# Kernel optimization log

Measured on AMD Instinct MI355X. Metric: run time of the kernel, lower is better.

The kernel has to match this reference:

```python
import jax, jax.numpy as jnp
import numpy as np

FRAC_BIT = 12
SCALE = float(2 ** FRAC_BIT)          # 12 fractional bits
QMIN, QMAX = -32768.0, 32767.0        # signed 16-bit two's complement range


def quant16(x):
    """Quantize to signed 16-bit fixed point with 12 fractional bits.

    Matches float_to_16bits_tensor / bit_slice semantics: the bit-serial
    crossbar MVM of the sliced operands equals an exact integer product of
    these fixed-point values, rescaled back to float.
    """
    return jnp.clip(jnp.round(x * SCALE), QMIN, QMAX) / SCALE


def setup_inputs() -> dict:
    key = jax.random.key(0)
    k1, k2 = jax.random.split(key)
    x = jax.random.normal(k1, (32, 128, 56, 56), dtype=jnp.float32)
    # kaiming-ish scale so weights are well inside the fixed-point range
    weight = jax.random.normal(k2, (256, 128, 3, 3), dtype=jnp.float32) * 0.05
    return {"x": x, "weight": weight}


def reference(x, weight):
    # The nested i/j loop in the original slides a stride-1 window over the
    # zero-padded input, performing a bit-sliced crossbar MVM per pixel.
    # That is exactly conv2d(stride=1, padding=1) on 16-bit fixed-point
    # quantized input and weight (bias row in the crossbar is zero / unused).
    qx = quant16(x)
    qw = quant16(weight)
    out = jax.lax.conv_general_dilated(
        qx, qw,
        window_strides=(1, 1),
        padding=((1, 1), (1, 1)),
        dimension_numbers=("NCHW", "OIHW", "NCHW"),
    )
    return out
```

## Files before the change

kernel.cpp:

```cpp
#include <hip/hip_runtime.h>
#include <cstdint>
#include <cstddef>


typedef __attribute__((ext_vector_type(8))) short short8;
typedef __attribute__((ext_vector_type(4))) float floatx4;

#define NIMG 32
#define CIN  128
#define HW   56
#define KOUT 256
#define HP   58
#define XPAD_ELEMS ((size_t)NIMG * HP * HP * CIN)
#define WT_OFF_BYTES (XPAD_ELEMS * 2)
#define KK 1152

__device__ __forceinline__ uint16_t quant_bf16(float v) {
    float q = rintf(v * 4096.0f);
    q = fminf(fmaxf(q, -32768.0f), 32767.0f) * (1.0f / 4096.0f);
    union { float f; uint32_t u; } cv; cv.f = q;
    uint32_t u = cv.u;
    return (uint16_t)((u + 0x7fffu + ((u >> 16) & 1u)) >> 16);
}

__global__ __launch_bounds__(256) void quant_pad_x(const float* __restrict__ x,
                                                   uint16_t* __restrict__ xp) {
    const int b = blockIdx.x;
    const int n = b / HW, h = b - n * HW;
    __shared__ uint16_t tile[HW * 130];
    const float* src = x + (size_t)n * CIN * HW * HW + (size_t)h * HW;
    for (int t = threadIdx.x; t < CIN * HW; t += 256) {
        int c = t / HW, w = t - c * HW;
        tile[w * 130 + c] = quant_bf16(src[(size_t)c * (HW * HW) + w]);
    }
    __syncthreads();
    uint32_t* dst = (uint32_t*)(xp + ((size_t)(n * HP + h + 1) * HP + 1) * CIN);
    for (int t = threadIdx.x; t < (HW * CIN) / 2; t += 256) {
        int w = t >> 6;
        int c2 = t & 63;
        uint32_t lo = tile[w * 130 + c2 * 2];
        uint32_t hi = tile[w * 130 + c2 * 2 + 1];
        dst[t] = lo | (hi << 16);
    }
}

__global__ __launch_bounds__(256) void quant_w(const float* __restrict__ w,
                                               uint16_t* __restrict__ wt) {
    int i = blockIdx.x * 256 + threadIdx.x;
    int k = i / KK;
    int r = i - k * KK;
    int tap = r >> 7;
    int c = r & 127;
    wt[i] = quant_bf16(w[(size_t)(k * CIN + c) * 9 + tap]);
}

__global__ __launch_bounds__(256) void conv_gemm(const uint16_t* __restrict__ xp,
                                                 const uint16_t* __restrict__ wt,
                                                 float* __restrict__ out) {
    __shared__ __align__(16) uint16_t As[128 * 32];
    __shared__ __align__(16) uint16_t Bs[128 * 32];

    const int tid = threadIdx.x;
    const int l   = tid & 63;
    const int wv  = tid >> 6;
    const int wr  = wv >> 1;
    const int wc  = wv & 1;
    const int kblk  = blockIdx.x;
    const int pxblk = blockIdx.y;

    const int chunk = l & 3;
    const int sub   = l >> 2;

    const uint16_t* aG[2];
    const uint16_t* bG[2];
#pragma unroll
    for (int i = 0; i < 2; ++i) {
        int row = wv * 32 + i * 16 + sub;
        aG[i] = wt + (size_t)(kblk * 128 + row) * KK + chunk * 8;
        int p = pxblk * 128 + row;
        int n = p / 3136; int rem = p - n * 3136;
        int hh = rem / HW; int ww = rem - hh * HW;
        bG[i] = xp + (size_t)((n * HP + hh) * HP + ww) * CIN + chunk * 8;
    }

    floatx4 acc[4][4];
#pragma unroll
    for (int a = 0; a < 4; ++a)
#pragma unroll
        for (int b = 0; b < 4; ++b)
            acc[a][b] = (floatx4){0.f, 0.f, 0.f, 0.f};

    const int m16 = l & 15;
    const int q   = l >> 4;

    for (int tap = 0; tap < 9; ++tap) {
        const int toff = (tap / 3) * HP + (tap % 3);
#pragma unroll
        for (int c4 = 0; c4 < 4; ++c4) {
            const int kt = tap * 4 + c4;
#pragma unroll
            for (int i = 0; i < 2; ++i) {
                __builtin_amdgcn_global_load_lds(
                    (__attribute__((address_space(1))) void*)(void*)(aG[i] + kt * 32),
                    (__attribute__((address_space(3))) void*)(void*)(&As[wv * 1024 + i * 512]),
                    16, 0, 0);
                __builtin_amdgcn_global_load_lds(
                    (__attribute__((address_space(1))) void*)(void*)(bG[i] + toff * CIN + c4 * 32),
                    (__attribute__((address_space(3))) void*)(void*)(&Bs[wv * 1024 + i * 512]),
                    16, 0, 0);
            }
            __syncthreads();
            short8 af[4], bf[4];
#pragma unroll
            for (int f = 0; f < 4; ++f) {
                af[f] = *(const short8*)&As[(wr * 64 + f * 16 + m16) * 32 + q * 8];
                bf[f] = *(const short8*)&Bs[(wc * 64 + f * 16 + m16) * 32 + q * 8];
            }
#pragma unroll
            for (int fr = 0; fr < 4; ++fr)
#pragma unroll
                for (int fc = 0; fc < 4; ++fc)
                    acc[fr][fc] = __builtin_amdgcn_mfma_f32_16x16x32_bf16(
                        af[fr], bf[fc], acc[fr][fc], 0, 0, 0);
            __syncthreads();
        }
    }

#pragma unroll
    for (int fc = 0; fc < 4; ++fc) {
        int p = pxblk * 128 + wc * 64 + fc * 16 + m16;
        int n = p / 3136; int rem = p - n * 3136;
        float* op = out + (size_t)(n * KOUT + kblk * 128) * 3136 + rem;
#pragma unroll
        for (int fr = 0; fr < 4; ++fr) {
            int kl = wr * 64 + fr * 16 + q * 4;
#pragma unroll
            for (int t = 0; t < 4; ++t)
                op[(size_t)(kl + t) * 3136] = acc[fr][fc][t];
        }
    }
}

extern "C" void kernel_launch(void* const* d_in, const int* in_sizes, int n_in,
                              void* d_out, int out_size, void* d_ws, size_t ws_size,
                              hipStream_t stream) {
    const float* x = (const float*)d_in[0];
    const float* w = (const float*)d_in[1];
    float* out = (float*)d_out;

    uint16_t* xp  = (uint16_t*)d_ws;
    uint16_t* wtb = (uint16_t*)((char*)d_ws + WT_OFF_BYTES);

    hipMemsetAsync(d_ws, 0, WT_OFF_BYTES, stream);
    quant_pad_x<<<NIMG * HW, 256, 0, stream>>>(x, xp);
    quant_w<<<(KOUT * KK) / 256, 256, 0, stream>>>(w, wtb);

    dim3 grid(2, 784);
    conv_gemm<<<grid, 256, 0, stream>>>(xp, wtb, out);
}
```

Baseline: 234.0 us.

## Fold padding into quant kernel, vectorize loads, swizzle LDS tiles

Removes the separate memset of the padded input buffer by having the quantize kernel write the zero border rows and columns itself, and widens its global loads and stores to float4 and uint2. In the GEMM kernel, the 16-byte chunks of each LDS row are XOR-swizzled on the global-to-LDS copy and un-swizzled on the fragment reads, to reduce LDS bank conflicts. The swizzle must stay consistent between the writing and reading lanes, otherwise results are wrong.

Result: faster. 227.7 us (-2.7%).

```diff
diff --git a/kernel.cpp b/kernel.cpp
--- a/kernel.cpp
+++ b/kernel.cpp
@@ -26,21 +26,39 @@
 __global__ __launch_bounds__(256) void quant_pad_x(const float* __restrict__ x,
                                                    uint16_t* __restrict__ xp) {
     const int b = blockIdx.x;
-    const int n = b / HW, h = b - n * HW;
+    const int n = b / HP, hp = b - n * HP;
+    uint16_t* row = xp + (size_t)(n * HP + hp) * HP * CIN;
+
+    if (hp == 0 || hp == HP - 1) {
+        uint4 z{0, 0, 0, 0};
+        uint4* d = (uint4*)row;
+        for (int t = threadIdx.x; t < HP * CIN * 2 / 16; t += 256) d[t] = z;
+        return;
+    }
+    const int h = hp - 1;
     __shared__ uint16_t tile[HW * 130];
     const float* src = x + (size_t)n * CIN * HW * HW + (size_t)h * HW;
-    for (int t = threadIdx.x; t < CIN * HW; t += 256) {
-        int c = t / HW, w = t - c * HW;
-        tile[w * 130 + c] = quant_bf16(src[(size_t)c * (HW * HW) + w]);
+    for (int t = threadIdx.x; t < CIN * 14; t += 256) {
+        int c = t / 14, w4 = t - c * 14;
+        float4 v = *(const float4*)(src + (size_t)c * (HW * HW) + w4 * 4);
+        int base = (w4 * 4) * 130 + c;
+        tile[base]       = quant_bf16(v.x);
+        tile[base + 130] = quant_bf16(v.y);
+        tile[base + 260] = quant_bf16(v.z);
+        tile[base + 390] = quant_bf16(v.w);
     }
     __syncthreads();
-    uint32_t* dst = (uint32_t*)(xp + ((size_t)(n * HP + h + 1) * HP + 1) * CIN);
-    for (int t = threadIdx.x; t < (HW * CIN) / 2; t += 256) {
-        int w = t >> 6;
-        int c2 = t & 63;
-        uint32_t lo = tile[w * 130 + c2 * 2];
-        uint32_t hi = tile[w * 130 + c2 * 2 + 1];
-        dst[t] = lo | (hi << 16);
+    if (threadIdx.x < 32) {
+        uint4 z{0, 0, 0, 0};
+        if (threadIdx.x < 16) ((uint4*)row)[threadIdx.x] = z;
+        else ((uint4*)(row + 57 * CIN))[threadIdx.x - 16] = z;
+    }
+    uint2* dst = (uint2*)(row + CIN);
+    for (int t = threadIdx.x; t < (HW * CIN) / 4; t += 256) {
+        int w = t >> 5, c4 = (t & 31) * 4;
+        uint32_t a = tile[w * 130 + c4]     | ((uint32_t)tile[w * 130 + c4 + 1] << 16);
+        uint32_t c = tile[w * 130 + c4 + 2] | ((uint32_t)tile[w * 130 + c4 + 3] << 16);
+        dst[t] = make_uint2(a, c);
     }
 }
 
@@ -68,19 +86,19 @@
     const int kblk  = blockIdx.x;
     const int pxblk = blockIdx.y;
 
-    const int chunk = l & 3;
-    const int sub   = l >> 2;
+    const int sub    = l >> 2;
+    const int c_data = (l & 3) ^ ((l >> 4) & 3);
 
     const uint16_t* aG[2];
     const uint16_t* bG[2];
 #pragma unroll
     for (int i = 0; i < 2; ++i) {
         int row = wv * 32 + i * 16 + sub;
-        aG[i] = wt + (size_t)(kblk * 128 + row) * KK + chunk * 8;
+        aG[i] = wt + (size_t)(kblk * 128 + row) * KK + c_data * 8;
         int p = pxblk * 128 + row;
         int n = p / 3136; int rem = p - n * 3136;
         int hh = rem / HW; int ww = rem - hh * HW;
-        bG[i] = xp + (size_t)((n * HP + hh) * HP + ww) * CIN + chunk * 8;
+        bG[i] = xp + (size_t)((n * HP + hh) * HP + ww) * CIN + c_data * 8;
     }
 
     floatx4 acc[4][4];
@@ -90,8 +108,9 @@
         for (int b = 0; b < 4; ++b)
             acc[a][b] = (floatx4){0.f, 0.f, 0.f, 0.f};
 
-    const int m16 = l & 15;
-    const int q   = l >> 4;
+    const int m16  = l & 15;
+    const int q    = l >> 4;
+    const int slot = (q ^ ((m16 >> 2) & 3)) * 8;
 
     for (int tap = 0; tap < 9; ++tap) {
         const int toff = (tap / 3) * HP + (tap % 3);
@@ -113,8 +132,8 @@
             short8 af[4], bf[4];
 #pragma unroll
             for (int f = 0; f < 4; ++f) {
-                af[f] = *(const short8*)&As[(wr * 64 + f * 16 + m16) * 32 + q * 8];
-                bf[f] = *(const short8*)&Bs[(wc * 64 + f * 16 + m16) * 32 + q * 8];
+                af[f] = *(const short8*)&As[(wr * 64 + f * 16 + m16) * 32 + slot];
+                bf[f] = *(const short8*)&Bs[(wc * 64 + f * 16 + m16) * 32 + slot];
             }
 #pragma unroll
             for (int fr = 0; fr < 4; ++fr)
@@ -151,8 +170,7 @@
     uint16_t* xp  = (uint16_t*)d_ws;
     uint16_t* wtb = (uint16_t*)((char*)d_ws + WT_OFF_BYTES);
 
-    hipMemsetAsync(d_ws, 0, WT_OFF_BYTES, stream);
-    quant_pad_x<<<NIMG * HW, 256, 0, stream>>>(x, xp);
+    quant_pad_x<<<NIMG * HP, 256, 0, stream>>>(x, xp);
     quant_w<<<(KOUT * KK) / 256, 256, 0, stream>>>(w, wtb);
 
     dim3 grid(2, 784);
```
